# Kernel optimization log

Measured on AMD Instinct MI355X. Metric: run time of the kernel, lower is better.

Reference implementation:

```python
import jax, jax.numpy as jnp
import numpy as np
from jax import lax

PATCH = 16  # get_patch patch_size; crop taken deterministically at (0,0) (original uses random offsets)
K = 5       # predicted kernel size (kernel_v.view(b,5,5))


def setup_inputs() -> dict:
    key = jax.random.key(0)
    ks = jax.random.split(key, 6)
    B, Cf, H, W = 16, 32, 64, 64
    Ci, Hi, Wi = 3, 512, 512
    return {
        "feature": jax.random.normal(ks[0], (B, Cf, H, W), dtype=jnp.float32),
        "img": jax.random.normal(ks[1], (B, Ci, Hi, Wi), dtype=jnp.float32),
        "conv_w": jax.random.normal(ks[2], (16, 32, 16, 16), dtype=jnp.float32) * 0.02,
        "conv_b": jax.random.normal(ks[3], (16,), dtype=jnp.float32) * 0.02,
        "lin_w": jax.random.normal(ks[4], (25, 144), dtype=jnp.float32) * 0.05,
        "lin_b": jax.random.normal(ks[5], (25,), dtype=jnp.float32) * 0.05,
    }


def reference(feature, img, conv_w, conv_b, lin_w, lin_b):
    B, C, H, W = img.shape
    # --- kernel predictor (eval mode: dropout is identity) ---
    patch = feature[:, :, :PATCH, :PATCH]  # deterministic top-left 16x16 crop
    f = lax.conv_general_dilated(
        patch, conv_w, window_strides=(1, 1), padding=[(1, 1), (1, 1)],
        dimension_numbers=("NCHW", "OIHW", "NCHW"))
    f = f + conv_b[None, :, None, None]            # [B,16,3,3]
    f = f.reshape(B, -1)                           # flatten -> [B,144]
    f = jax.nn.gelu(f, approximate=False)          # torch GELU default = exact erf
    kernel_v = f @ lin_w.T + lin_b                 # [B,25]
    # --- per-sample 5x5 filtering (kornia.filter2D: reflect pad, correlation,
    #     same kernel broadcast over channels) fused as one grouped depthwise conv ---
    k = jnp.broadcast_to(kernel_v.reshape(B, 1, K, K), (B, C, K, K)).reshape(B * C, 1, K, K)
    pad = K // 2
    xp = jnp.pad(img, ((0, 0), (0, 0), (pad, pad), (pad, pad)), mode="reflect")
    xp = xp.reshape(1, B * C, H + 2 * pad, W + 2 * pad)
    out = lax.conv_general_dilated(
        xp, k, window_strides=(1, 1), padding="VALID",
        feature_group_count=B * C,
        dimension_numbers=("NCHW", "OIHW", "NCHW"))
    return out.reshape(B, C, H, W)
```

## Files before the change

### kernel.cpp

```cpp
#include <hip/hip_runtime.h>
#include <math.h>


#define B_  16
#define C_  3
#define H_  512
#define W_  512

__global__ __launch_bounds__(256) void patch_conv_kernel(
    const float* __restrict__ feature,
    const float* __restrict__ conv_w,
    const float* __restrict__ conv_b,
    float* __restrict__ g_out)
{
    __shared__ float patch_raw[17 + 8192 + 17];
    __shared__ float red[9][4];
    float* patch = patch_raw + 17;

    int blk = blockIdx.x;
    int b   = blk >> 4;
    int oc  = blk & 15;
    int tid = threadIdx.x;

    const float* fb = feature + (size_t)b * 32 * 4096;
    const float* wb = conv_w + (size_t)oc * 8192;

    if (tid < 17) { patch_raw[tid] = 0.f; patch_raw[17 + 8192 + tid] = 0.f; }

    for (int i = tid; i < 8192; i += 256) {
        int ic = i >> 8;
        int r  = i & 255;
        patch[i] = fb[ic * 4096 + (r >> 4) * 64 + (r & 15)];
    }

    float wreg[32];
    #pragma unroll
    for (int ic = 0; ic < 32; ic++) wreg[ic] = wb[ic * 256 + tid];

    __syncthreads();

    int kh = tid >> 4;
    int kw = tid & 15;

    float acc[9];
    #pragma unroll
    for (int k = 0; k < 9; k++) acc[k] = 0.f;

    #pragma unroll 4
    for (int ic = 0; ic < 32; ic++) {
        int base = ic * 256 + tid;
        float wv = wreg[ic];
        #pragma unroll
        for (int di = 0; di < 3; di++) {
            #pragma unroll
            for (int dj = 0; dj < 3; dj++) {
                acc[di * 3 + dj] += patch[base + (di - 1) * 16 + (dj - 1)] * wv;
            }
        }
    }

    #pragma unroll
    for (int di = 0; di < 3; di++) {
        #pragma unroll
        for (int dj = 0; dj < 3; dj++) {
            bool ok = ((unsigned)(kh + di - 1) < 16u) &&
                      ((unsigned)(kw + dj - 1) < 16u);
            if (!ok) acc[di * 3 + dj] = 0.f;
        }
    }

    #pragma unroll
    for (int k = 0; k < 9; k++) {
        float v = acc[k];
        #pragma unroll
        for (int off = 32; off > 0; off >>= 1)
            v += __shfl_xor(v, off, 64);
        acc[k] = v;
    }
    int wid  = tid >> 6;
    int lane = tid & 63;
    if (lane == 0) {
        #pragma unroll
        for (int k = 0; k < 9; k++) red[k][wid] = acc[k];
    }
    __syncthreads();
    if (tid < 9) {
        float s = red[tid][0] + red[tid][1] + red[tid][2] + red[tid][3];
        s += conv_b[oc];
        float g = 0.5f * s * (1.0f + erff(s * 0.70710678118654752f));
        g_out[(b * 16 + oc) * 9 + tid] = g;
    }
}

__global__ __launch_bounds__(256) void kv_kernel(
    const float* __restrict__ g_in,
    const float* __restrict__ lin_w,
    const float* __restrict__ lin_b,
    float* __restrict__ kv_out)
{
    __shared__ float wsh[25 * 144];
    __shared__ float gsh[144];
    int b   = blockIdx.x;
    int tid = threadIdx.x;

    for (int i = tid; i < 25 * 144; i += 256) wsh[i] = lin_w[i];
    if (tid < 144) gsh[tid] = g_in[b * 144 + tid];
    __syncthreads();

    if (tid < 25) {
        float acc = lin_b[tid];
        #pragma unroll 8
        for (int j = 0; j < 144; j++) acc += gsh[j] * wsh[tid * 144 + j];
        kv_out[b * 25 + tid] = acc;
    }
}

#define TS   64
#define ITS  68

__device__ __forceinline__ int reflect_idx(int v, int n) {
    v = (v < 0) ? -v : v;
    v = (v >= n) ? (2 * n - 2 - v) : v;
    return v;
}

__global__ __launch_bounds__(256) void depthwise_kernel(
    const float* __restrict__ img,
    const float* __restrict__ kv,
    float* __restrict__ out)
{
    __shared__ float tile_s[ITS * ITS];

    int bc   = blockIdx.y;
    int b    = bc / C_;
    int tile = blockIdx.x;
    int tyi  = tile >> 3;
    int txi  = tile & 7;
    int ty0  = tyi * TS;
    int tx0  = txi * TS;

    int tid = threadIdx.x;

    float w[25];
    {
        const float* kvp = kv + b * 25;
        #pragma unroll
        for (int i = 0; i < 25; i++) w[i] = kvp[i];
    }

    const float* ip = img + (size_t)bc * H_ * W_;
    float* op       = out + (size_t)bc * H_ * W_;

    int tx = (tid & 15) * 4;
    int ty = (tid >> 4) * 4;

    float acc[4][4];
    #pragma unroll
    for (int i = 0; i < 4; i++)
        #pragma unroll
        for (int j = 0; j < 4; j++) acc[i][j] = 0.f;

    bool interior = (tyi >= 1) && (tyi <= 6) && (txi >= 1) && (txi <= 6);

    if (interior) {
        const float* base = ip + (size_t)(ty0 + ty - 2) * W_ + (tx0 + tx);
        #pragma unroll
        for (int r = 0; r < 8; r++) {
            const float* rp = base + r * W_;
            float2 a = *(const float2*)(rp - 2);
            float4 m = *(const float4*)(rp);
            float2 c = *(const float2*)(rp + 4);
            float x[8] = {a.x, a.y, m.x, m.y, m.z, m.w, c.x, c.y};
            #pragma unroll
            for (int orow = 0; orow < 4; orow++) {
                int dy = r - orow;
                if (dy >= 0 && dy < 5) {
                    #pragma unroll
                    for (int dx = 0; dx < 5; dx++) {
                        float wv = w[dy * 5 + dx];
                        #pragma unroll
                        for (int oc = 0; oc < 4; oc++)
                            acc[orow][oc] += wv * x[oc + dx];
                    }
                }
            }
        }
    } else {
        bool xedge = (txi == 0) || (txi == 7);
        for (int i = tid; i < ITS * 34; i += 256) {
            int ly = i / 34;
            int c  = i - ly * 34;
            int gy = reflect_idx(ty0 + ly - 2, H_);
            int gx = tx0 + 2 * c - 2;
            const float* rowp = ip + gy * W_;
            float2 v;
            if (!xedge || (unsigned)gx < (unsigned)(W_ - 1)) {
                v = *(const float2*)&rowp[gx];
            } else {
                v.x = rowp[reflect_idx(gx, W_)];
                v.y = rowp[reflect_idx(gx + 1, W_)];
            }
            *(float2*)&tile_s[ly * ITS + 2 * c] = v;
        }
        __syncthreads();

        #pragma unroll
        for (int r = 0; r < 8; r++) {
            const float* rowp = &tile_s[(ty + r) * ITS + tx];
            float4 a = *(const float4*)rowp;
            float4 bb = *(const float4*)(rowp + 4);
            float x[8] = {a.x, a.y, a.z, a.w, bb.x, bb.y, bb.z, bb.w};
            #pragma unroll
            for (int orow = 0; orow < 4; orow++) {
                int dy = r - orow;
                if (dy >= 0 && dy < 5) {
                    #pragma unroll
                    for (int dx = 0; dx < 5; dx++) {
                        float wv = w[dy * 5 + dx];
                        #pragma unroll
                        for (int oc = 0; oc < 4; oc++)
                            acc[orow][oc] += wv * x[oc + dx];
                    }
                }
            }
        }
    }

    #pragma unroll
    for (int orow = 0; orow < 4; orow++) {
        float4 o;
        o.x = acc[orow][0]; o.y = acc[orow][1];
        o.z = acc[orow][2]; o.w = acc[orow][3];
        *(float4*)&op[(ty0 + ty + orow) * W_ + tx0 + tx] = o;
    }
}

extern "C" void kernel_launch(void* const* d_in, const int* in_sizes, int n_in,
                              void* d_out, int out_size, void* d_ws, size_t ws_size,
                              hipStream_t stream) {
    const float* feature = (const float*)d_in[0];
    const float* img     = (const float*)d_in[1];
    const float* conv_w  = (const float*)d_in[2];
    const float* conv_b  = (const float*)d_in[3];
    const float* lin_w   = (const float*)d_in[4];
    const float* lin_b   = (const float*)d_in[5];
    float* out = (float*)d_out;

    float* g_ws  = (float*)d_ws;
    float* kv_ws = g_ws + 2304;

    patch_conv_kernel<<<B_ * 16, 256, 0, stream>>>(feature, conv_w, conv_b, g_ws);
    kv_kernel<<<B_, 256, 0, stream>>>(g_ws, lin_w, lin_b, kv_ws);

    dim3 grid(64, B_ * C_);
    depthwise_kernel<<<grid, 256, 0, stream>>>(img, kv_ws, out);
}
```

Before: 136.6 us.

## Register-streamed depthwise tiles of 8 rows, drop shared-memory edge path

The depthwise 5x5 filter now has each thread compute 8 output rows by 4 columns. It streams input rows through a 4-row rotating register window, which cuts the vertical halo overhead from 8/4 to 12/8 rows per output. The shared-memory edge path is removed: reflection is handled per row index and with precomputed column indices, and a template splits the x-interior and x-edge cases. Kernel weights are made wave-uniform with readfirstlane, and the grid is halved to 32 tiles per channel image. The risks are higher register pressure and fewer blocks.

```diff
diff --git a/kernel.cpp b/kernel.cpp
--- a/kernel.cpp
+++ b/kernel.cpp
@@ -115,8 +115,8 @@
     }
 }
 
-#define TS   64
-#define ITS  68
+#define TSX  64
+#define TSY  128
 
 __device__ __forceinline__ int reflect_idx(int v, int n) {
     v = (v < 0) ? -v : v;
@@ -124,115 +124,122 @@
     return v;
 }
 
+template <bool XFAST>
+__device__ __forceinline__ void dw_tile(
+    const float* __restrict__ ip, float* __restrict__ op,
+    const float* w, int ty0, int tx0, int tx, int tyl)
+{
+    int gx0 = tx0 + tx;
+    int xid[8];
+    if (!XFAST) {
+        #pragma unroll
+        for (int j = 0; j < 8; j++) xid[j] = reflect_idx(gx0 - 2 + j, W_);
+    }
+
+    float acc[8][4];
+    #pragma unroll
+    for (int i = 0; i < 8; i++)
+        #pragma unroll
+        for (int j = 0; j < 4; j++) acc[i][j] = 0.f;
+
+    float win[4][8];
+
+    #pragma unroll
+    for (int r = 0; r < 4; r++) {
+        int gy = reflect_idx(ty0 + tyl + r - 2, H_);
+        const float* rowp = ip + (size_t)gy * W_;
+        if (XFAST) {
+            const float* rp = rowp + gx0;
+            float2 a = *(const float2*)(rp - 2);
+            float4 m = *(const float4*)(rp);
+            float2 c = *(const float2*)(rp + 4);
+            win[r][0] = a.x; win[r][1] = a.y;
+            win[r][2] = m.x; win[r][3] = m.y; win[r][4] = m.z; win[r][5] = m.w;
+            win[r][6] = c.x; win[r][7] = c.y;
+        } else {
+            #pragma unroll
+            for (int j = 0; j < 8; j++) win[r][j] = rowp[xid[j]];
+        }
+    }
+
+    #pragma unroll
+    for (int r = 0; r < 12; r++) {
+        const float* x = win[r & 3];
+        #pragma unroll
+        for (int orow = 0; orow < 8; orow++) {
+            int dy = r - orow;
+            if (dy >= 0 && dy < 5) {
+                #pragma unroll
+                for (int dx = 0; dx < 5; dx++) {
+                    float wv = w[dy * 5 + dx];
+                    #pragma unroll
+                    for (int oc = 0; oc < 4; oc++)
+                        acc[orow][oc] += wv * x[oc + dx];
+                }
+            }
+        }
+        if (r + 4 < 12) {
+            int rn = r + 4;
+            int gy = reflect_idx(ty0 + tyl + rn - 2, H_);
+            const float* rowp = ip + (size_t)gy * W_;
+            float* wdst = win[r & 3];
+            if (XFAST) {
+                const float* rp = rowp + gx0;
+                float2 a = *(const float2*)(rp - 2);
+                float4 m = *(const float4*)(rp);
+                float2 c = *(const float2*)(rp + 4);
+                wdst[0] = a.x; wdst[1] = a.y;
+                wdst[2] = m.x; wdst[3] = m.y; wdst[4] = m.z; wdst[5] = m.w;
+                wdst[6] = c.x; wdst[7] = c.y;
+            } else {
+                #pragma unroll
+                for (int j = 0; j < 8; j++) wdst[j] = rowp[xid[j]];
+            }
+        }
+    }
+
+    #pragma unroll
+    for (int orow = 0; orow < 8; orow++) {
+        float4 o;
+        o.x = acc[orow][0]; o.y = acc[orow][1];
+        o.z = acc[orow][2]; o.w = acc[orow][3];
+        *(float4*)&op[(size_t)(ty0 + tyl + orow) * W_ + gx0] = o;
+    }
+}
+
 __global__ __launch_bounds__(256) void depthwise_kernel(
     const float* __restrict__ img,
     const float* __restrict__ kv,
     float* __restrict__ out)
 {
-    __shared__ float tile_s[ITS * ITS];
-
     int bc   = blockIdx.y;
     int b    = bc / C_;
     int tile = blockIdx.x;
     int tyi  = tile >> 3;
     int txi  = tile & 7;
-    int ty0  = tyi * TS;
-    int tx0  = txi * TS;
+    int ty0  = tyi * TSY;
+    int tx0  = txi * TSX;
 
     int tid = threadIdx.x;
+    int tx  = (tid & 15) * 4;
+    int tyl = (tid >> 4) * 8;
 
     float w[25];
     {
         const float* kvp = kv + b * 25;
         #pragma unroll
-        for (int i = 0; i < 25; i++) w[i] = kvp[i];
+        for (int i = 0; i < 25; i++)
+            w[i] = __int_as_float(
+                __builtin_amdgcn_readfirstlane(__float_as_int(kvp[i])));
     }
 
     const float* ip = img + (size_t)bc * H_ * W_;
     float* op       = out + (size_t)bc * H_ * W_;
 
-    int tx = (tid & 15) * 4;
-    int ty = (tid >> 4) * 4;
-
-    float acc[4][4];
-    #pragma unroll
-    for (int i = 0; i < 4; i++)
-        #pragma unroll
-        for (int j = 0; j < 4; j++) acc[i][j] = 0.f;
-
-    bool interior = (tyi >= 1) && (tyi <= 6) && (txi >= 1) && (txi <= 6);
-
-    if (interior) {
-        const float* base = ip + (size_t)(ty0 + ty - 2) * W_ + (tx0 + tx);
-        #pragma unroll
-        for (int r = 0; r < 8; r++) {
-            const float* rp = base + r * W_;
-            float2 a = *(const float2*)(rp - 2);
-            float4 m = *(const float4*)(rp);
-            float2 c = *(const float2*)(rp + 4);
-            float x[8] = {a.x, a.y, m.x, m.y, m.z, m.w, c.x, c.y};
-            #pragma unroll
-            for (int orow = 0; orow < 4; orow++) {
-                int dy = r - orow;
-                if (dy >= 0 && dy < 5) {
-                    #pragma unroll
-                    for (int dx = 0; dx < 5; dx++) {
-                        float wv = w[dy * 5 + dx];
-                        #pragma unroll
-                        for (int oc = 0; oc < 4; oc++)
-                            acc[orow][oc] += wv * x[oc + dx];
-                    }
-                }
-            }
-        }
-    } else {
-        bool xedge = (txi == 0) || (txi == 7);
-        for (int i = tid; i < ITS * 34; i += 256) {
-            int ly = i / 34;
-            int c  = i - ly * 34;
-            int gy = reflect_idx(ty0 + ly - 2, H_);
-            int gx = tx0 + 2 * c - 2;
-            const float* rowp = ip + gy * W_;
-            float2 v;
-            if (!xedge || (unsigned)gx < (unsigned)(W_ - 1)) {
-                v = *(const float2*)&rowp[gx];
-            } else {
-                v.x = rowp[reflect_idx(gx, W_)];
-                v.y = rowp[reflect_idx(gx + 1, W_)];
-            }
-            *(float2*)&tile_s[ly * ITS + 2 * c] = v;
-        }
-        __syncthreads();
-
-        #pragma unroll
-        for (int r = 0; r < 8; r++) {
-            const float* rowp = &tile_s[(ty + r) * ITS + tx];
-            float4 a = *(const float4*)rowp;
-            float4 bb = *(const float4*)(rowp + 4);
-            float x[8] = {a.x, a.y, a.z, a.w, bb.x, bb.y, bb.z, bb.w};
-            #pragma unroll
-            for (int orow = 0; orow < 4; orow++) {
-                int dy = r - orow;
-                if (dy >= 0 && dy < 5) {
-                    #pragma unroll
-                    for (int dx = 0; dx < 5; dx++) {
-                        float wv = w[dy * 5 + dx];
-                        #pragma unroll
-                        for (int oc = 0; oc < 4; oc++)
-                            acc[orow][oc] += wv * x[oc + dx];
-                    }
-                }
-            }
-        }
-    }
-
-    #pragma unroll
-    for (int orow = 0; orow < 4; orow++) {
-        float4 o;
-        o.x = acc[orow][0]; o.y = acc[orow][1];
-        o.z = acc[orow][2]; o.w = acc[orow][3];
-        *(float4*)&op[(ty0 + ty + orow) * W_ + tx0 + tx] = o;
-    }
+    if (txi >= 1 && txi <= 6)
+        dw_tile<true >(ip, op, w, ty0, tx0, tx, tyl);
+    else
+        dw_tile<false>(ip, op, w, ty0, tx0, tx, tyl);
 }
 
 extern "C" void kernel_launch(void* const* d_in, const int* in_sizes, int n_in,
@@ -252,6 +259,6 @@
     patch_conv_kernel<<<B_ * 16, 256, 0, stream>>>(feature, conv_w, conv_b, g_ws);
     kv_kernel<<<B_, 256, 0, stream>>>(g_ws, lin_w, lin_b, kv_ws);
 
-    dim3 grid(64, B_ * C_);
+    dim3 grid(32, B_ * C_);
     depthwise_kernel<<<grid, 256, 0, stream>>>(img, kv_ws, out);
 }
```

After: 132.7 us. 2.9% less time.
